# Kernel optimization log

Hardware: AMD Instinct MI355X
Metric: run time of the kernel (lower is better)

## Reference

```python
import jax, jax.numpy as jnp
import numpy as np

NY, NU, NHIDDEN = 64, 64, 256
NHRZ, NBATCH = 1024, 128


def setup_inputs() -> dict:
    key = jax.random.key(0)
    ks = jax.random.split(key, 9)
    y0 = jax.random.normal(ks[0], (NBATCH, NY), dtype=jnp.float32)
    U = jax.random.normal(ks[1], (NHRZ, NBATCH, NU), dtype=jnp.float32)
    # parameters (match torch init: uniform(0,1) for continuous eigen params,
    # randn/sqrt(Nu) for B, Kaiming-uniform-ish for Linear layers)
    lmbd_cont_real = jax.random.uniform(ks[2], (NHIDDEN // 2,), dtype=jnp.float32)
    lmbd_cont_imag = jax.random.uniform(ks[3], (NHIDDEN // 2,), dtype=jnp.float32)
    B = jax.random.normal(ks[4], (NHIDDEN, NU), dtype=jnp.float32) / np.sqrt(NU)
    lim1 = 1.0 / np.sqrt(NY)
    W_y2x = jax.random.uniform(ks[5], (NHIDDEN, NY), dtype=jnp.float32, minval=-lim1, maxval=lim1)
    b_y2x = jax.random.uniform(ks[6], (NHIDDEN,), dtype=jnp.float32, minval=-lim1, maxval=lim1)
    lim2 = 1.0 / np.sqrt(NHIDDEN)
    W_x2y = jax.random.uniform(ks[7], (NY, NHIDDEN), dtype=jnp.float32, minval=-lim2, maxval=lim2)
    b_x2y = jax.random.uniform(ks[8], (NY,), dtype=jnp.float32, minval=-lim2, maxval=lim2)
    return {"y0": y0, "U": U, "lmbd_cont_real": lmbd_cont_real,
            "lmbd_cont_imag": lmbd_cont_imag, "B": B,
            "W_y2x": W_y2x, "b_y2x": b_y2x, "W_x2y": W_x2y, "b_x2y": b_x2y}


def reference(y0, U, lmbd_cont_real, lmbd_cont_imag, B, W_y2x, b_y2x, W_x2y, b_x2y):
    n = lmbd_cont_real.shape[0]  # Nhidden // 2
    r = jnp.exp(-jnp.abs(lmbd_cont_real))
    theta = (np.pi / 2.0) * lmbd_cont_imag
    lmbd_real = r * jnp.cos(theta)  # [n]
    lmbd_imag = r * jnp.sin(theta)  # [n]
    nf = jnp.sqrt(1.0 - jnp.exp(-2.0 * jnp.abs(lmbd_cont_real)))
    nf = jnp.concatenate([nf, nf])  # [Nhidden]
    # Bu[t,b,h] = (U @ B^T) * nf
    Bu = jnp.einsum('tbu,hu->tbh', U, B) * nf  # [Nhrz, Nbatch, Nhidden]
    x0 = y0 @ W_y2x.T + b_y2x  # [Nbatch, Nhidden]

    # x @ A^T with A = [[diag(lr), -diag(li)], [diag(li), diag(lr)]] is a
    # per-pair 2x2 rotation -> pure elementwise ops (same math, no dense matmul)
    def step(x, bu):
        x1, x2 = x[:, :n], x[:, n:]
        xn = jnp.concatenate([lmbd_real * x1 - lmbd_imag * x2,
                              lmbd_imag * x1 + lmbd_real * x2], axis=-1) + bu
        return xn, xn

    _, X = jax.lax.scan(step, x0, Bu)  # X: [Nhrz, Nbatch, Nhidden]
    Y = X @ W_x2y.T + b_x2y  # [Nhrz, Nbatch, Ny]
    return Y
```

## Files before the change

kernel.cpp:

```cpp
#include <hip/hip_runtime.h>
#include <hip/hip_bf16.h>
#include <stdint.h>

#define T_HRZ 1024
#define NBAT  128
#define NHID  256
#define NPAIR 128
#define NUIN  64
#define NYOUT 64
#define LCH   16
#define CCH   64
#define GCH   4
#define NGRP  16

#define WS_LAM   0
#define WS_LAML  256
#define WS_X0P   512
#define WS_WBU   33280
#define WS_WBY   41472
#define WS_S     49664

#define X16_PITCH 264
#define XA_SB 136
#define XA_SK 552

typedef __attribute__((ext_vector_type(8))) short short8;
typedef __attribute__((ext_vector_type(4))) float float4v;

union Frag { short8 s8; unsigned int u32[4]; };

__device__ __forceinline__ unsigned int f2bf_bits(float x) {
  unsigned int u = __float_as_uint(x);
  return (u + 0x7fffu + ((u >> 16) & 1u)) >> 16;
}

__device__ __forceinline__ unsigned int pkbf(float a, float b) {
  __hip_bfloat162 h = __float22bfloat162_rn(make_float2(a, b));
  union { __hip_bfloat162 h2; unsigned int u; } cv; cv.h2 = h; return cv.u;
}

__global__ __launch_bounds__(256) void k_prep(
    const float* __restrict__ y0, const float* __restrict__ lrc,
    const float* __restrict__ lic, const float* __restrict__ Bm,
    const float* __restrict__ Wy2x, const float* __restrict__ by2x,
    const float* __restrict__ Wx2y, float* __restrict__ ws)
{
  int blk = blockIdx.x;
  int h = threadIdx.x;
  if (blk < NBAT) {
    __shared__ float y0s[NYOUT];
    if (h < NYOUT) y0s[h] = y0[blk * NYOUT + h];
    __syncthreads();
    float acc = by2x[h];
    const float* wr = Wy2x + h * NYOUT;
#pragma unroll 16
    for (int k = 0; k < NYOUT; ++k) acc += y0s[k] * wr[k];
    int j = h & (NPAIR - 1);
    int comp = h >> 7;
    ws[WS_X0P + (blk * NPAIR + j) * 2 + comp] = acc;
  } else if (blk == NBAT) {
    if (h < NPAIR) {
      float a  = fabsf(lrc[h]);
      float r  = expf(-a);
      float th = 1.5707963267948966f * lic[h];
      float lr = r * cosf(th);
      float li = r * sinf(th);
      ws[WS_LAM + h]         = lr;
      ws[WS_LAM + NPAIR + h] = li;
      float pr = lr, pi_ = li;
      for (int l = 1; l < LCH; ++l) {
        float nr = pr * lr - pi_ * li;
        float ni = pr * li + pi_ * lr;
        pr = nr; pi_ = ni;
      }
      ws[WS_LAML + h]         = pr;
      ws[WS_LAML + NPAIR + h] = pi_;
    }
  } else if (blk == NBAT + 1) {
    unsigned short* wbu = (unsigned short*)(ws + WS_WBU);
    for (int idx = h; idx < 16384; idx += 256) {
      int nt   = idx >> 10;
      int kk   = (idx >> 9) & 1;
      int lane = (idx >> 3) & 63;
      int jj   = idx & 7;
      int u  = kk * 32 + (lane >> 4) * 8 + jj;
      int hh = nt * 16 + (lane & 15);
      float a2 = fabsf(lrc[hh & (NPAIR - 1)]);
      float nf = sqrtf(1.f - expf(-2.f * a2));
      wbu[idx] = (unsigned short)f2bf_bits(Bm[hh * NUIN + u] * nf);
    }
  } else {
    unsigned short* wby = (unsigned short*)(ws + WS_WBY);
    for (int idx = h; idx < 16384; idx += 256) {
      int nt   = idx >> 12;
      int kk   = (idx >> 9) & 7;
      int lane = (idx >> 3) & 63;
      int jj   = idx & 7;
      int hh = kk * 32 + (lane >> 4) * 8 + jj;
      int y  = nt * 16 + (lane & 15);
      wby[idx] = (unsigned short)f2bf_bits(Wx2y[y * NHID + hh]);
    }
  }
}

__global__ __launch_bounds__(128, 4) void k_pass1(
    const float* __restrict__ U, float* __restrict__ ws)
{
  __shared__ unsigned short X16s[LCH * X16_PITCH];
  int tid = threadIdx.x, wave = tid >> 6, lane = tid & 63;
  int l15 = lane & 15, q = lane >> 4;
  int b = blockIdx.x, g = blockIdx.y;

  int j = tid;
  float lr = ws[WS_LAM + j], li = ws[WS_LAM + NPAIR + j];

  const short8* wbu = (const short8*)(ws + WS_WBU);
  float4v z = {0.f, 0.f, 0.f, 0.f};
  float S1 = 0.f, S2 = 0.f;

#pragma unroll
  for (int k = 0; k < GCH; ++k) {
    int c = g * GCH + k;
    const float* urow = U + ((size_t)(c * LCH + l15) * NBAT + b) * NUIN;
    Frag afr[2];
#pragma unroll
    for (int kk = 0; kk < 2; ++kk) {
      int u0 = kk * 32 + q * 8;
      float4 va = *(const float4*)(urow + u0);
      float4 vb = *(const float4*)(urow + u0 + 4);
      afr[kk].u32[0] = pkbf(va.x, va.y);
      afr[kk].u32[1] = pkbf(va.z, va.w);
      afr[kk].u32[2] = pkbf(vb.x, vb.y);
      afr[kk].u32[3] = pkbf(vb.z, vb.w);
    }
    float4v acc[8];
#pragma unroll
    for (int n = 0; n < 8; ++n) acc[n] = z;
#pragma unroll
    for (int n = 0; n < 8; ++n) {
      int nt = wave * 8 + n;
      acc[n] = __builtin_amdgcn_mfma_f32_16x16x32_bf16(afr[0].s8, wbu[(nt * 2 + 0) * 64 + lane], acc[n], 0, 0, 0);
      acc[n] = __builtin_amdgcn_mfma_f32_16x16x32_bf16(afr[1].s8, wbu[(nt * 2 + 1) * 64 + lane], acc[n], 0, 0, 0);
    }
#pragma unroll
    for (int n = 0; n < 8; ++n) {
      int hh = (wave * 8 + n) * 16 + l15;
      int off = (hh & 127) * 2 + (hh >> 7);
#pragma unroll
      for (int r = 0; r < 4; ++r)
        X16s[(q * 4 + r) * X16_PITCH + off] = (unsigned short)f2bf_bits(acc[n][r]);
    }
    __syncthreads();
#pragma unroll
    for (int l = 0; l < LCH; ++l) {
      unsigned int pkv = *(const unsigned int*)(X16s + l * X16_PITCH + j * 2);
      float v1 = __uint_as_float(pkv << 16);
      float v2 = __uint_as_float(pkv & 0xffff0000u);
      float n1 = lr * S1 - li * S2 + v1;
      float n2 = li * S1 + lr * S2 + v2;
      S1 = n1; S2 = n2;
    }
    if (k < GCH - 1) __syncthreads();
  }

  ((float2*)(ws + WS_S))[((size_t)g * NBAT + b) * NPAIR + j] = make_float2(S1, S2);
}

__global__ __launch_bounds__(128, 4) void k_pass2(
    const float* __restrict__ U, const float* __restrict__ bx2y,
    float* __restrict__ out, float* __restrict__ ws)
{
  __shared__ unsigned short X16s[LCH * X16_PITCH];
  __shared__ unsigned short XAs[8 * XA_SK];
  int tid = threadIdx.x, wave = tid >> 6, lane = tid & 63;
  int l15 = lane & 15, q = lane >> 4;
  int b = blockIdx.x, g = blockIdx.y;

  int j = tid;
  float lr = ws[WS_LAM + j], li = ws[WS_LAM + NPAIR + j];
  float L16r = ws[WS_LAML + j], L16i = ws[WS_LAML + NPAIR + j];
  float L32r = L16r * L16r - L16i * L16i, L32i = 2.f * L16r * L16i;
  float L64r = L32r * L32r - L32i * L32i, L64i = 2.f * L32r * L32i;

  float e1 = ws[WS_X0P + (b * NPAIR + j) * 2 + 0];
  float e2 = ws[WS_X0P + (b * NPAIR + j) * 2 + 1];
  {
    const float2* sp = (const float2*)(ws + WS_S);
#pragma unroll
    for (int g2 = 0; g2 < NGRP - 1; ++g2)
      if (g2 < g) {
        float2 s = sp[((size_t)g2 * NBAT + b) * NPAIR + j];
        float n1 = L64r * e1 - L64i * e2 + s.x;
        float n2 = L64i * e1 + L64r * e2 + s.y;
        e1 = n1; e2 = n2;
      }
  }

  const short8* wbu = (const short8*)(ws + WS_WBU);
  const short8* wby = (const short8*)(ws + WS_WBY);
  float4v z = {0.f, 0.f, 0.f, 0.f};
  int base1 = (j >> 5) * XA_SK       + ((j >> 3) & 3) * XA_SB + (j & 7);
  int base2 = ((j >> 5) + 4) * XA_SK + ((j >> 3) & 3) * XA_SB + (j & 7);
  float x1 = e1, x2 = e2;
  float bias0 = bx2y[(wave * 2 + 0) * 16 + l15];
  float bias1 = bx2y[(wave * 2 + 1) * 16 + l15];

#pragma unroll
  for (int k = 0; k < GCH; ++k) {
    int c = g * GCH + k;
    const float* urow = U + ((size_t)(c * LCH + l15) * NBAT + b) * NUIN;
    Frag afr[2];
#pragma unroll
    for (int kk = 0; kk < 2; ++kk) {
      int u0 = kk * 32 + q * 8;
      float4 va = *(const float4*)(urow + u0);
      float4 vb = *(const float4*)(urow + u0 + 4);
      afr[kk].u32[0] = pkbf(va.x, va.y);
      afr[kk].u32[1] = pkbf(va.z, va.w);
      afr[kk].u32[2] = pkbf(vb.x, vb.y);
      afr[kk].u32[3] = pkbf(vb.z, vb.w);
    }
    float4v acc[8];
#pragma unroll
    for (int n = 0; n < 8; ++n) acc[n] = z;
#pragma unroll
    for (int n = 0; n < 8; ++n) {
      int nt = wave * 8 + n;
      acc[n] = __builtin_amdgcn_mfma_f32_16x16x32_bf16(afr[0].s8, wbu[(nt * 2 + 0) * 64 + lane], acc[n], 0, 0, 0);
      acc[n] = __builtin_amdgcn_mfma_f32_16x16x32_bf16(afr[1].s8, wbu[(nt * 2 + 1) * 64 + lane], acc[n], 0, 0, 0);
    }
#pragma unroll
    for (int n = 0; n < 8; ++n) {
      int hh = (wave * 8 + n) * 16 + l15;
      int off = (hh & 127) * 2 + (hh >> 7);
#pragma unroll
      for (int r = 0; r < 4; ++r)
        X16s[(q * 4 + r) * X16_PITCH + off] = (unsigned short)f2bf_bits(acc[n][r]);
    }
    __syncthreads();
#pragma unroll
    for (int l = 0; l < LCH; ++l) {
      unsigned int pkv = *(const unsigned int*)(X16s + l * X16_PITCH + j * 2);
      float v1 = __uint_as_float(pkv << 16);
      float v2 = __uint_as_float(pkv & 0xffff0000u);
      float n1 = lr * x1 - li * x2 + v1;
      float n2 = li * x1 + lr * x2 + v2;
      x1 = n1; x2 = n2;
      XAs[base1 + l * 8] = (unsigned short)f2bf_bits(x1);
      XAs[base2 + l * 8] = (unsigned short)f2bf_bits(x2);
    }
    __syncthreads();
    float4v acc0 = z, acc1 = z;
    int nt0 = wave * 2, nt1 = nt0 + 1;
#pragma unroll
    for (int kk = 0; kk < 8; ++kk) {
      short8 a = *(const short8*)(XAs + kk * XA_SK + q * XA_SB + l15 * 8);
      acc0 = __builtin_amdgcn_mfma_f32_16x16x32_bf16(a, wby[(nt0 * 8 + kk) * 64 + lane], acc0, 0, 0, 0);
      acc1 = __builtin_amdgcn_mfma_f32_16x16x32_bf16(a, wby[(nt1 * 8 + kk) * 64 + lane], acc1, 0, 0, 0);
    }
#pragma unroll
    for (int r = 0; r < 4; ++r) {
      int row = q * 4 + r;
      size_t o = ((size_t)(c * LCH + row) * NBAT + b) * NYOUT;
      out[o + nt0 * 16 + l15] = acc0[r] + bias0;
      out[o + nt1 * 16 + l15] = acc1[r] + bias1;
    }
  }
}

extern "C" void kernel_launch(void* const* d_in, const int* in_sizes, int n_in,
                              void* d_out, int out_size, void* d_ws, size_t ws_size,
                              hipStream_t stream) {
  (void)in_sizes; (void)n_in; (void)out_size; (void)ws_size;
  const float* y0   = (const float*)d_in[0];
  const float* U    = (const float*)d_in[1];
  const float* lrc  = (const float*)d_in[2];
  const float* lic  = (const float*)d_in[3];
  const float* Bm   = (const float*)d_in[4];
  const float* Wy2x = (const float*)d_in[5];
  const float* by2x = (const float*)d_in[6];
  const float* Wx2y = (const float*)d_in[7];
  const float* bx2y = (const float*)d_in[8];
  float* out = (float*)d_out;
  float* ws  = (float*)d_ws;

  k_prep<<<dim3(NBAT + 3), 256, 0, stream>>>(y0, lrc, lic, Bm, Wy2x, by2x, Wx2y, ws);
  k_pass1<<<dim3(NBAT, NGRP - 1), 128, 0, stream>>>(U, ws);
  k_pass2<<<dim3(NBAT, NGRP), 128, 0, stream>>>(U, bx2y, out, ws);
}
```

Before: 152.0 us.

## Store packed Bu in workspace in pass1 and reuse it in pass2

Pass1 now runs one block per 16-step chunk across all 64 chunks instead of 4-chunk groups. It computes the U·Bᵀ projection once and writes the packed bf16 Bu pairs to a global workspace buffer along with per-chunk end states. Pass2 drops its own U load and MFMA projection and reads the packed Bu back from global memory. It also composes the carried-in state chunk by chunk using the λ^16 factor. This removes the duplicated projection matmul and the U read in pass2, but adds about 64 MB of workspace writes and reads plus a longer serial prefix scan in pass2.

```diff
diff --git a/kernel.cpp b/kernel.cpp
--- a/kernel.cpp
+++ b/kernel.cpp
@@ -19,6 +19,7 @@
 #define WS_WBU   33280
 #define WS_WBY   41472
 #define WS_S     49664
+#define WS_BUPK  2146816
 
 #define X16_PITCH 264
 #define XA_SB 136
@@ -109,94 +110,95 @@
   __shared__ unsigned short X16s[LCH * X16_PITCH];
   int tid = threadIdx.x, wave = tid >> 6, lane = tid & 63;
   int l15 = lane & 15, q = lane >> 4;
-  int b = blockIdx.x, g = blockIdx.y;
+  int b = blockIdx.x, c = blockIdx.y;
 
   int j = tid;
   float lr = ws[WS_LAM + j], li = ws[WS_LAM + NPAIR + j];
 
   const short8* wbu = (const short8*)(ws + WS_WBU);
   float4v z = {0.f, 0.f, 0.f, 0.f};
+
+  const float* urow = U + ((size_t)(c * LCH + l15) * NBAT + b) * NUIN;
+  Frag afr[2];
+#pragma unroll
+  for (int kk = 0; kk < 2; ++kk) {
+    int u0 = kk * 32 + q * 8;
+    float4 va = *(const float4*)(urow + u0);
+    float4 vb = *(const float4*)(urow + u0 + 4);
+    afr[kk].u32[0] = pkbf(va.x, va.y);
+    afr[kk].u32[1] = pkbf(va.z, va.w);
+    afr[kk].u32[2] = pkbf(vb.x, vb.y);
+    afr[kk].u32[3] = pkbf(vb.z, vb.w);
+  }
+  float4v acc[8];
+#pragma unroll
+  for (int n = 0; n < 8; ++n) acc[n] = z;
+#pragma unroll
+  for (int n = 0; n < 8; ++n) {
+    int nt = wave * 8 + n;
+    acc[n] = __builtin_amdgcn_mfma_f32_16x16x32_bf16(afr[0].s8, wbu[(nt * 2 + 0) * 64 + lane], acc[n], 0, 0, 0);
+    acc[n] = __builtin_amdgcn_mfma_f32_16x16x32_bf16(afr[1].s8, wbu[(nt * 2 + 1) * 64 + lane], acc[n], 0, 0, 0);
+  }
+#pragma unroll
+  for (int n = 0; n < 8; ++n) {
+    int hh = (wave * 8 + n) * 16 + l15;
+    int off = (hh & 127) * 2 + (hh >> 7);
+#pragma unroll
+    for (int r = 0; r < 4; ++r)
+      X16s[(q * 4 + r) * X16_PITCH + off] = (unsigned short)f2bf_bits(acc[n][r]);
+  }
+  __syncthreads();
+
+  unsigned int* bupk = (unsigned int*)(ws + WS_BUPK);
   float S1 = 0.f, S2 = 0.f;
-
-#pragma unroll
-  for (int k = 0; k < GCH; ++k) {
-    int c = g * GCH + k;
-    const float* urow = U + ((size_t)(c * LCH + l15) * NBAT + b) * NUIN;
-    Frag afr[2];
-#pragma unroll
-    for (int kk = 0; kk < 2; ++kk) {
-      int u0 = kk * 32 + q * 8;
-      float4 va = *(const float4*)(urow + u0);
-      float4 vb = *(const float4*)(urow + u0 + 4);
-      afr[kk].u32[0] = pkbf(va.x, va.y);
-      afr[kk].u32[1] = pkbf(va.z, va.w);
-      afr[kk].u32[2] = pkbf(vb.x, vb.y);
-      afr[kk].u32[3] = pkbf(vb.z, vb.w);
-    }
-    float4v acc[8];
-#pragma unroll
-    for (int n = 0; n < 8; ++n) acc[n] = z;
-#pragma unroll
-    for (int n = 0; n < 8; ++n) {
-      int nt = wave * 8 + n;
-      acc[n] = __builtin_amdgcn_mfma_f32_16x16x32_bf16(afr[0].s8, wbu[(nt * 2 + 0) * 64 + lane], acc[n], 0, 0, 0);
-      acc[n] = __builtin_amdgcn_mfma_f32_16x16x32_bf16(afr[1].s8, wbu[(nt * 2 + 1) * 64 + lane], acc[n], 0, 0, 0);
-    }
-#pragma unroll
-    for (int n = 0; n < 8; ++n) {
-      int hh = (wave * 8 + n) * 16 + l15;
-      int off = (hh & 127) * 2 + (hh >> 7);
-#pragma unroll
-      for (int r = 0; r < 4; ++r)
-        X16s[(q * 4 + r) * X16_PITCH + off] = (unsigned short)f2bf_bits(acc[n][r]);
-    }
-    __syncthreads();
-#pragma unroll
-    for (int l = 0; l < LCH; ++l) {
-      unsigned int pkv = *(const unsigned int*)(X16s + l * X16_PITCH + j * 2);
-      float v1 = __uint_as_float(pkv << 16);
-      float v2 = __uint_as_float(pkv & 0xffff0000u);
-      float n1 = lr * S1 - li * S2 + v1;
-      float n2 = li * S1 + lr * S2 + v2;
-      S1 = n1; S2 = n2;
-    }
-    if (k < GCH - 1) __syncthreads();
-  }
-
-  ((float2*)(ws + WS_S))[((size_t)g * NBAT + b) * NPAIR + j] = make_float2(S1, S2);
+#pragma unroll
+  for (int l = 0; l < LCH; ++l) {
+    unsigned int pkv = *(const unsigned int*)(X16s + l * X16_PITCH + j * 2);
+    bupk[((size_t)(c * LCH + l) * NBAT + b) * NPAIR + j] = pkv;
+    float v1 = __uint_as_float(pkv << 16);
+    float v2 = __uint_as_float(pkv & 0xffff0000u);
+    float n1 = lr * S1 - li * S2 + v1;
+    float n2 = li * S1 + lr * S2 + v2;
+    S1 = n1; S2 = n2;
+  }
+  ((float2*)(ws + WS_S))[((size_t)c * NBAT + b) * NPAIR + j] = make_float2(S1, S2);
 }
 
 __global__ __launch_bounds__(128, 4) void k_pass2(
-    const float* __restrict__ U, const float* __restrict__ bx2y,
-    float* __restrict__ out, float* __restrict__ ws)
+    const float* __restrict__ bx2y, float* __restrict__ out,
+    float* __restrict__ ws)
 {
-  __shared__ unsigned short X16s[LCH * X16_PITCH];
   __shared__ unsigned short XAs[8 * XA_SK];
   int tid = threadIdx.x, wave = tid >> 6, lane = tid & 63;
   int l15 = lane & 15, q = lane >> 4;
   int b = blockIdx.x, g = blockIdx.y;
 
   int j = tid;
-  float lr = ws[WS_LAM + j], li = ws[WS_LAM + NPAIR + j];
+  float lr = ws[WS_LAM + j],  li = ws[WS_LAM + NPAIR + j];
   float L16r = ws[WS_LAML + j], L16i = ws[WS_LAML + NPAIR + j];
-  float L32r = L16r * L16r - L16i * L16i, L32i = 2.f * L16r * L16i;
-  float L64r = L32r * L32r - L32i * L32i, L64i = 2.f * L32r * L32i;
 
   float e1 = ws[WS_X0P + (b * NPAIR + j) * 2 + 0];
   float e2 = ws[WS_X0P + (b * NPAIR + j) * 2 + 1];
   {
     const float2* sp = (const float2*)(ws + WS_S);
-#pragma unroll
-    for (int g2 = 0; g2 < NGRP - 1; ++g2)
-      if (g2 < g) {
-        float2 s = sp[((size_t)g2 * NBAT + b) * NPAIR + j];
-        float n1 = L64r * e1 - L64i * e2 + s.x;
-        float n2 = L64i * e1 + L64r * e2 + s.y;
-        e1 = n1; e2 = n2;
-      }
-  }
-
-  const short8* wbu = (const short8*)(ws + WS_WBU);
+    size_t o0 = (size_t)b * NPAIR + j;
+    int nc = g * GCH;
+    for (int c2 = 0; c2 < nc; c2 += 8) {
+      float2 v[8];
+#pragma unroll
+      for (int t = 0; t < 8; ++t)
+        if (c2 + t < nc) v[t] = sp[(size_t)(c2 + t) * (NBAT * NPAIR) + o0];
+#pragma unroll
+      for (int t = 0; t < 8; ++t)
+        if (c2 + t < nc) {
+          float n1 = L16r * e1 - L16i * e2 + v[t].x;
+          float n2 = L16i * e1 + L16r * e2 + v[t].y;
+          e1 = n1; e2 = n2;
+        }
+    }
+  }
+
+  const unsigned int* bupk = (const unsigned int*)(ws + WS_BUPK);
   const short8* wby = (const short8*)(ws + WS_WBY);
   float4v z = {0.f, 0.f, 0.f, 0.f};
   int base1 = (j >> 5) * XA_SK       + ((j >> 3) & 3) * XA_SB + (j & 7);
@@ -208,41 +210,14 @@
 #pragma unroll
   for (int k = 0; k < GCH; ++k) {
     int c = g * GCH + k;
-    const float* urow = U + ((size_t)(c * LCH + l15) * NBAT + b) * NUIN;
-    Frag afr[2];
-#pragma unroll
-    for (int kk = 0; kk < 2; ++kk) {
-      int u0 = kk * 32 + q * 8;
-      float4 va = *(const float4*)(urow + u0);
-      float4 vb = *(const float4*)(urow + u0 + 4);
-      afr[kk].u32[0] = pkbf(va.x, va.y);
-      afr[kk].u32[1] = pkbf(va.z, va.w);
-      afr[kk].u32[2] = pkbf(vb.x, vb.y);
-      afr[kk].u32[3] = pkbf(vb.z, vb.w);
-    }
-    float4v acc[8];
-#pragma unroll
-    for (int n = 0; n < 8; ++n) acc[n] = z;
-#pragma unroll
-    for (int n = 0; n < 8; ++n) {
-      int nt = wave * 8 + n;
-      acc[n] = __builtin_amdgcn_mfma_f32_16x16x32_bf16(afr[0].s8, wbu[(nt * 2 + 0) * 64 + lane], acc[n], 0, 0, 0);
-      acc[n] = __builtin_amdgcn_mfma_f32_16x16x32_bf16(afr[1].s8, wbu[(nt * 2 + 1) * 64 + lane], acc[n], 0, 0, 0);
-    }
-#pragma unroll
-    for (int n = 0; n < 8; ++n) {
-      int hh = (wave * 8 + n) * 16 + l15;
-      int off = (hh & 127) * 2 + (hh >> 7);
-#pragma unroll
-      for (int r = 0; r < 4; ++r)
-        X16s[(q * 4 + r) * X16_PITCH + off] = (unsigned short)f2bf_bits(acc[n][r]);
-    }
-    __syncthreads();
+    unsigned int pk[LCH];
+#pragma unroll
+    for (int l = 0; l < LCH; ++l)
+      pk[l] = bupk[((size_t)(c * LCH + l) * NBAT + b) * NPAIR + j];
 #pragma unroll
     for (int l = 0; l < LCH; ++l) {
-      unsigned int pkv = *(const unsigned int*)(X16s + l * X16_PITCH + j * 2);
-      float v1 = __uint_as_float(pkv << 16);
-      float v2 = __uint_as_float(pkv & 0xffff0000u);
+      float v1 = __uint_as_float(pk[l] << 16);
+      float v2 = __uint_as_float(pk[l] & 0xffff0000u);
       float n1 = lr * x1 - li * x2 + v1;
       float n2 = li * x1 + lr * x2 + v2;
       x1 = n1; x2 = n2;
@@ -265,6 +240,7 @@
       out[o + nt0 * 16 + l15] = acc0[r] + bias0;
       out[o + nt1 * 16 + l15] = acc1[r] + bias1;
     }
+    if (k < GCH - 1) __syncthreads();
   }
 }
 
@@ -285,6 +261,6 @@
   float* ws  = (float*)d_ws;
 
   k_prep<<<dim3(NBAT + 3), 256, 0, stream>>>(y0, lrc, lic, Bm, Wy2x, by2x, Wx2y, ws);
-  k_pass1<<<dim3(NBAT, NGRP - 1), 128, 0, stream>>>(U, ws);
-  k_pass2<<<dim3(NBAT, NGRP), 128, 0, stream>>>(U, bx2y, out, ws);
-}
+  k_pass1<<<dim3(NBAT, CCH), 128, 0, stream>>>(U, ws);
+  k_pass2<<<dim3(NBAT, NGRP), 128, 0, stream>>>(bx2y, out, ws);
+}
```

Measured after the change: 148.1 us. 1.03x faster.
